# Kernel tuning notes

Measured on AMD Instinct MI355X. Metric: run time of the kernel, lower is better.

## Reference

```python
import jax, jax.numpy as jnp
import numpy as np

DIM = 1  # quantization axis (channels)


def setup_inputs() -> dict:
    key = jax.random.key(0)
    kx, kc = jax.random.split(key)
    x = jax.random.normal(kx, (32, 256, 32, 32), dtype=jnp.float32)
    # nn.init.normal_(weight, 0, 1.1)
    codebook = 1.1 * jax.random.normal(kc, (8192, 256), dtype=jnp.float32)
    return {"x": x, "codebook": codebook}


def reference(x, codebook):
    # move quantization dim to last: [B, C, H, W] -> [B, W, H, C]
    xt = jnp.swapaxes(x, -1, DIM)
    flat = xt.reshape(-1, xt.shape[-1])  # [N, D]
    # squared distances ||f - c||^2 = ||f||^2 - 2 f.c + ||c||^2  -> [N, K]
    d2 = (jnp.sum(flat * flat, axis=1, keepdims=True)
          - 2.0 * (flat @ codebook.T)
          + jnp.sum(codebook * codebook, axis=1))
    idx = jnp.argmin(d2, axis=1)                      # [N]
    codes = codebook[idx].reshape(xt.shape)           # nearest-code gather
    indices = idx.reshape(xt.shape[:-1])
    # transpose back to original layout
    codes = jnp.swapaxes(codes, -1, DIM)              # [B, C, H, W]
    indices = jnp.swapaxes(indices, -1, DIM)          # [B, H, W]
    return codes, indices
```

## Files before the change

kernel.cpp:

```cpp
#include <hip/hip_runtime.h>
#include <math.h>


typedef _Float16 v8h __attribute__((ext_vector_type(8)));
typedef float f32x16 __attribute__((ext_vector_type(16)));
typedef unsigned int u32;

#define MFMA16 __builtin_amdgcn_mfma_f32_32x32x16_f16

__device__ __forceinline__ void gll16(const _Float16* g, _Float16* l) {
  __builtin_amdgcn_global_load_lds(
      (const __attribute__((address_space(1))) void*)(const void*)g,
      (__attribute__((address_space(3))) void*)(void*)l, 16, 0, 0);
}

__global__ __launch_bounds__(256) void cnorm_k(const float4* __restrict__ cb4,
                                               float* __restrict__ cn) {
  int lane = threadIdx.x & 63;
  int row = (blockIdx.x << 2) + (threadIdx.x >> 6);
  float4 v = cb4[(size_t)row * 64 + lane];
  float s = v.x * v.x + v.y * v.y + v.z * v.z + v.w * v.w;
#pragma unroll
  for (int off = 32; off > 0; off >>= 1) s += __shfl_xor(s, off, 64);
  if (lane == 0) cn[row] = s;
}

__global__ __launch_bounds__(256) void split_cb(const float4* __restrict__ cb4,
                                                _Float16* __restrict__ W) {
  const int j = threadIdx.x & 31;
  const int ks = j >> 1, hi = j & 1;
  const int r = (blockIdx.x << 3) + (threadIdx.x >> 5);
  const float4* src = cb4 + (size_t)r * 64 + (ks << 2) + (hi << 1);
  float4 v0 = src[0], v1 = src[1];
  float t[8] = {v0.x, v0.y, v0.z, v0.w, v1.x, v1.y, v1.z, v1.w};
  v8h hv, mv;
#pragma unroll
  for (int i = 0; i < 8; ++i) {
    float vs = t[i] * 8192.f;
    _Float16 h = (_Float16)vs;
    _Float16 m = (_Float16)(vs - (float)h);
    hv[i] = h; mv[i] = m;
  }
  const int wv = (r >> 6) & 7, c64 = r & 63;
  _Float16* base = W + ((size_t)((r >> 9) << 4) + ks) * 16384 + (wv << 11);
  *(v8h*)(base + (hi << 9) + (c64 << 3)) = hv;
  *(v8h*)(base + 1024 + (hi << 9) + (c64 << 3)) = mv;
}

__global__ void __launch_bounds__(512, 1) vq_fast(const float* __restrict__ x,
                                                  const float4* __restrict__ cb4,
                                                  const float* __restrict__ cn,
                                                  const _Float16* __restrict__ W,
                                                  float* __restrict__ out) {
  __shared__ __align__(16) _Float16 F2[2][64][264];
  __shared__ __align__(16) _Float16 Bsh[2][16384];
  __shared__ float fnP[64][8];
  __shared__ float fnS[64];
  __shared__ float wredS[8][64];
  __shared__ u32  wredC[8][64];
  __shared__ u32  finS[64];

  const int tid = threadIdx.x;
  const int lane = tid & 63;
  const int w = tid >> 6;
  const int col = lane & 31;
  const int hi = lane >> 5;
  const int b = blockIdx.x >> 4;
  const int h0 = (blockIdx.x & 15) << 1;

  const int chunk = w << 11;
  const int rb0 = chunk + (hi << 9) + (col << 3);

  {
    const _Float16* src = W + chunk + (lane << 3);
#pragma unroll
    for (int i = 0; i < 4; ++i) gll16(src + (i << 9), &Bsh[0][chunk + (i << 9)]);
  }

  {
    const float* xb = x + ((size_t)b << 18) + (h0 << 5);
    float s = 0.f;
#pragma unroll
    for (int j = 0; j < 4; ++j) {
      v8h hv, mv;
#pragma unroll
      for (int i = 0; i < 8; ++i) {
        const int c = (w << 5) + (j << 3) + i;
        float v = xb[(size_t)c * 1024 + lane];
        s += v * v;
        float vs = v * 8192.f;
        _Float16 h = (_Float16)vs;
        _Float16 m = (_Float16)(vs - (float)h);
        hv[i] = h; mv[i] = m;
      }
      *(v8h*)&F2[0][lane][(w << 5) + (j << 3)] = hv;
      *(v8h*)&F2[1][lane][(w << 5) + (j << 3)] = mv;
    }
    fnP[lane][w] = s;
  }
  __syncthreads();
  if (tid < 64) {
    float t = 0.f;
#pragma unroll
    for (int j = 0; j < 8; ++j) t += fnP[tid][j];
    fnS[tid] = t;
  }
  __syncthreads();

  if (w >= 4) __builtin_amdgcn_s_sleep(15);

  float fnr[32];
#pragma unroll
  for (int sl = 0; sl < 32; ++sl) {
    const int row = ((sl >> 4) << 5) + (sl & 3) + (((sl >> 2) & 3) << 3) + (hi << 2);
    fnr[sl] = fnS[row];
  }

  f32x16 a00, a01, a10, a11;
#pragma unroll
  for (int r = 0; r < 16; ++r) { a00[r] = 0.f; a01[r] = 0.f; a10[r] = 0.f; a11[r] = 0.f; }
  float mn[32];
#pragma unroll
  for (int sl = 0; sl < 32; ++sl) mn[sl] = INFINITY;
  u32 idp[8] = {0, 0, 0, 0, 0, 0, 0, 0};
  float cnv0 = 0.f, cnv1 = 0.f;

#pragma unroll 1
  for (int ct = 0; ct < 16; ++ct) {
    if (w >= 4) __builtin_amdgcn_s_sleep(1);
#pragma unroll
    for (int ks = 0; ks < 16; ++ks) {
      const int st = (ct << 4) + ks;
      if (ks == 0) {
        cnv0 = cn[(ct << 9) + (w << 6) + col];
        cnv1 = cn[(ct << 9) + (w << 6) + 32 + col];
      }
      const bool more = (ct < 15) || (ks < 15);
      if (more) {
        const _Float16* src = W + ((size_t)(st + 1) << 14) + chunk + (lane << 3);
        _Float16* dst = &Bsh[(st + 1) & 1][chunk];
#pragma unroll
        for (int i = 0; i < 4; ++i) gll16(src + (i << 9), dst + (i << 9));
      }
      if (more) asm volatile("s_waitcnt vmcnt(4)" ::: "memory");
      else      asm volatile("s_waitcnt vmcnt(0)" ::: "memory");
      __builtin_amdgcn_sched_barrier(0);

      const int ko = (ks << 4) + (hi << 3);
      const v8h ah0 = *(const v8h*)&F2[0][col][ko];
      const v8h ah1 = *(const v8h*)&F2[0][32 + col][ko];
      const v8h am0 = *(const v8h*)&F2[1][col][ko];
      const v8h am1 = *(const v8h*)&F2[1][32 + col][ko];
      const _Float16* Bb = Bsh[st & 1];
      const v8h bh0 = *(const v8h*)&Bb[rb0];
      const v8h bh1 = *(const v8h*)&Bb[rb0 + 256];
      const v8h bm0 = *(const v8h*)&Bb[rb0 + 1024];
      const v8h bm1 = *(const v8h*)&Bb[rb0 + 1280];

      a00 = MFMA16(ah0, bh0, a00, 0, 0, 0);
      a01 = MFMA16(ah0, bh1, a01, 0, 0, 0);
      a10 = MFMA16(ah1, bh0, a10, 0, 0, 0);
      a11 = MFMA16(ah1, bh1, a11, 0, 0, 0);
      a00 = MFMA16(ah0, bm0, a00, 0, 0, 0);
      a01 = MFMA16(ah0, bm1, a01, 0, 0, 0);
      a10 = MFMA16(ah1, bm0, a10, 0, 0, 0);
      a11 = MFMA16(ah1, bm1, a11, 0, 0, 0);
      a00 = MFMA16(am0, bh0, a00, 0, 0, 0);
      a01 = MFMA16(am0, bh1, a01, 0, 0, 0);
      a10 = MFMA16(am1, bh0, a10, 0, 0, 0);
      a11 = MFMA16(am1, bh1, a11, 0, 0, 0);
    }
#pragma unroll
    for (int sl = 0; sl < 32; ++sl) {
      const int Mb = sl >> 4, reg = sl & 15;
      const float base = fnr[sl];
      const u32 sh = (u32)((sl & 3) << 3);
      {
        const float d = (Mb == 0) ? a00[reg] : a10[reg];
        float s = (base + (-0x1p-25f) * d) + cnv0;
        const bool better = s < mn[sl];
        const u32 curv = idp[sl >> 2];
        const u32 upd = (curv & ~(255u << sh)) | (((u32)(ct << 1)) << sh);
        idp[sl >> 2] = better ? upd : curv;
        mn[sl] = better ? s : mn[sl];
      }
      {
        const float d = (Mb == 0) ? a01[reg] : a11[reg];
        float s = (base + (-0x1p-25f) * d) + cnv1;
        const bool better = s < mn[sl];
        const u32 curv = idp[sl >> 2];
        const u32 upd = (curv & ~(255u << sh)) | (((u32)((ct << 1) | 1)) << sh);
        idp[sl >> 2] = better ? upd : curv;
        mn[sl] = better ? s : mn[sl];
      }
    }
#pragma unroll
    for (int r = 0; r < 16; ++r) { a00[r] = 0.f; a01[r] = 0.f; a10[r] = 0.f; a11[r] = 0.f; }
  }

#pragma unroll
  for (int sl = 0; sl < 32; ++sl) {
    float v = mn[sl];
    const u32 byte = (idp[sl >> 2] >> ((sl & 3) << 3)) & 255u;
    u32 code = ((byte >> 1) << 9) + ((u32)w << 6) + ((byte & 1) << 5) + (u32)col;
#pragma unroll
    for (int off = 1; off < 32; off <<= 1) {
      float v2 = __shfl_xor(v, off, 64);
      u32 c2 = (u32)__shfl_xor((int)code, off, 64);
      if (v2 < v || (v2 == v && c2 < code)) { v = v2; code = c2; }
    }
    if (col == 0) {
      const int row = ((sl >> 4) << 5) + (sl & 3) + (((sl >> 2) & 3) << 3) + (hi << 2);
      wredS[w][row] = v; wredC[w][row] = code;
    }
  }
  __syncthreads();
  if (tid < 64) {
    float bv = wredS[0][tid]; u32 bc = wredC[0][tid];
#pragma unroll
    for (int j = 1; j < 8; ++j) {
      float vv = wredS[j][tid]; u32 cc = wredC[j][tid];
      if (vv < bv || (vv == bv && cc < bc)) { bv = vv; bc = cc; }
    }
    finS[tid] = bc;
    out[(size_t)8388608 + ((size_t)b << 10) + (h0 << 5) + tid] = (float)bc;
  }
  __syncthreads();

  {
    const int pt = tid & 63, cg = tid >> 6;
    const u32 code = finS[pt];
    const float4* cbr = cb4 + ((size_t)code << 6);
    const size_t obase = ((size_t)b << 18) + (h0 << 5) + pt;
#pragma unroll
    for (int cc = 0; cc < 8; ++cc) {
      const int c4 = (cc << 3) + cg;
      float4 vv = cbr[c4];
      out[obase + (size_t)((c4 << 2) + 0) * 1024] = vv.x;
      out[obase + (size_t)((c4 << 2) + 1) * 1024] = vv.y;
      out[obase + (size_t)((c4 << 2) + 2) * 1024] = vv.z;
      out[obase + (size_t)((c4 << 2) + 3) * 1024] = vv.w;
    }
  }
}

__global__ void __launch_bounds__(512, 2) vq_fb(const float* __restrict__ x,
                                                const float4* __restrict__ cb4,
                                                const float* __restrict__ cn,
                                                float* __restrict__ out) {
  __shared__ __align__(16) _Float16 F2[2][64][264];
  __shared__ __align__(16) _Float16 Bsh[512][72];
  __shared__ float fnP[64][8];
  __shared__ float fnS[64];
  __shared__ float wredS[8][64];
  __shared__ u32  wredC[8][64];
  __shared__ u32  finS[64];

  const int tid = threadIdx.x;
  const int lane = tid & 63;
  const int w = tid >> 6;
  const int col = lane & 31;
  const int hi = lane >> 5;
  const int b = blockIdx.x >> 4;
  const int h0 = (blockIdx.x & 15) << 1;

  float4 rg[8];
  {
    const float4* src = cb4 + ((size_t)tid << 6);
#pragma unroll
    for (int j = 0; j < 8; ++j) rg[j] = src[j];
  }
  {
    const float* xb = x + ((size_t)b << 18) + (h0 << 5);
    float s = 0.f;
#pragma unroll
    for (int j = 0; j < 4; ++j) {
      v8h hv, mv;
#pragma unroll
      for (int i = 0; i < 8; ++i) {
        const int c = (w << 5) + (j << 3) + i;
        float v = xb[(size_t)c * 1024 + lane];
        s += v * v;
        float vs = v * 8192.f;
        _Float16 h = (_Float16)vs;
        _Float16 m = (_Float16)(vs - (float)h);
        hv[i] = h; mv[i] = m;
      }
      *(v8h*)&F2[0][lane][(w << 5) + (j << 3)] = hv;
      *(v8h*)&F2[1][lane][(w << 5) + (j << 3)] = mv;
    }
    fnP[lane][w] = s;
  }
  __syncthreads();
  if (tid < 64) {
    float t = 0.f;
#pragma unroll
    for (int j = 0; j < 8; ++j) t += fnP[tid][j];
    fnS[tid] = t;
  }
  {
#pragma unroll
    for (int j = 0; j < 4; ++j) {
      float t0[8] = {rg[2*j].x, rg[2*j].y, rg[2*j].z, rg[2*j].w,
                     rg[2*j+1].x, rg[2*j+1].y, rg[2*j+1].z, rg[2*j+1].w};
      v8h hv, mv;
#pragma unroll
      for (int i = 0; i < 8; ++i) {
        float vs = t0[i] * 8192.f;
        _Float16 h = (_Float16)vs;
        _Float16 m = (_Float16)(vs - (float)h);
        hv[i] = h; mv[i] = m;
      }
      *(v8h*)&Bsh[tid][(j << 3)] = hv;
      *(v8h*)&Bsh[tid][32 + (j << 3)] = mv;
    }
  }
  __syncthreads();

  float fnr[32];
#pragma unroll
  for (int sl = 0; sl < 32; ++sl) {
    const int row = ((sl >> 4) << 5) + (sl & 3) + (((sl >> 2) & 3) << 3) + (hi << 2);
    fnr[sl] = fnS[row];
  }

  f32x16 acc[2][2];
#pragma unroll
  for (int r = 0; r < 16; ++r) {
    acc[0][0][r] = 0.f; acc[0][1][r] = 0.f; acc[1][0][r] = 0.f; acc[1][1][r] = 0.f;
  }
  float mn[32];
#pragma unroll
  for (int sl = 0; sl < 32; ++sl) mn[sl] = INFINITY;
  u32 idp[8] = {0, 0, 0, 0, 0, 0, 0, 0};
  float cnv0 = 0.f, cnv1 = 0.f;

  for (int st = 0; st < 128; ++st) {
    const int ks = st & 7, ct = st >> 3;
    if (st < 127) {
      const int tn = st + 1;
      const float4* src = cb4 + ((size_t)((((tn >> 3) << 9) + tid)) << 6) + ((tn & 7) << 3);
#pragma unroll
      for (int j = 0; j < 8; ++j) rg[j] = src[j];
    }
    if (ks == 0) {
      cnv0 = cn[(ct << 9) + (w << 6) + col];
      cnv1 = cn[(ct << 9) + (w << 6) + 32 + col];
    }
    const int kb = ks << 5;
#pragma unroll
    for (int kh = 0; kh < 2; ++kh) {
      const int ko = kb + (kh << 4) + (hi << 3);
      const v8h ah0 = *(const v8h*)&F2[0][col][ko];
      const v8h ah1 = *(const v8h*)&F2[0][32 + col][ko];
      const v8h am0 = *(const v8h*)&F2[1][col][ko];
      const v8h am1 = *(const v8h*)&F2[1][32 + col][ko];
      const int bo = (kh << 4) + (hi << 3);
      const v8h bh0 = *(const v8h*)&Bsh[(w << 6) + col][bo];
      const v8h bh1 = *(const v8h*)&Bsh[(w << 6) + 32 + col][bo];
      const v8h bm0 = *(const v8h*)&Bsh[(w << 6) + col][32 + bo];
      const v8h bm1 = *(const v8h*)&Bsh[(w << 6) + 32 + col][32 + bo];
      acc[0][0] = MFMA16(ah0, bh0, acc[0][0], 0, 0, 0);
      acc[0][0] = MFMA16(ah0, bm0, acc[0][0], 0, 0, 0);
      acc[0][0] = MFMA16(am0, bh0, acc[0][0], 0, 0, 0);
      acc[0][1] = MFMA16(ah0, bh1, acc[0][1], 0, 0, 0);
      acc[0][1] = MFMA16(ah0, bm1, acc[0][1], 0, 0, 0);
      acc[0][1] = MFMA16(am0, bh1, acc[0][1], 0, 0, 0);
      acc[1][0] = MFMA16(ah1, bh0, acc[1][0], 0, 0, 0);
      acc[1][0] = MFMA16(ah1, bm0, acc[1][0], 0, 0, 0);
      acc[1][0] = MFMA16(am1, bh0, acc[1][0], 0, 0, 0);
      acc[1][1] = MFMA16(ah1, bh1, acc[1][1], 0, 0, 0);
      acc[1][1] = MFMA16(ah1, bm1, acc[1][1], 0, 0, 0);
      acc[1][1] = MFMA16(am1, bh1, acc[1][1], 0, 0, 0);
    }
    if (ks == 7) {
#pragma unroll
      for (int sl = 0; sl < 32; ++sl) {
        const int Mb = sl >> 4, reg = sl & 15;
        const float base = fnr[sl];
        const u32 sh = (u32)((sl & 3) << 3);
        {
          float s = (base + (-0x1p-25f) * acc[Mb][0][reg]) + cnv0;
          const bool better = s < mn[sl];
          const u32 curv = idp[sl >> 2];
          const u32 upd = (curv & ~(255u << sh)) | (((u32)(ct << 1)) << sh);
          idp[sl >> 2] = better ? upd : curv;
          mn[sl] = better ? s : mn[sl];
        }
        {
          float s = (base + (-0x1p-25f) * acc[Mb][1][reg]) + cnv1;
          const bool better = s < mn[sl];
          const u32 curv = idp[sl >> 2];
          const u32 upd = (curv & ~(255u << sh)) | (((u32)((ct << 1) | 1)) << sh);
          idp[sl >> 2] = better ? upd : curv;
          mn[sl] = better ? s : mn[sl];
        }
      }
#pragma unroll
      for (int r = 0; r < 16; ++r) {
        acc[0][0][r] = 0.f; acc[0][1][r] = 0.f; acc[1][0][r] = 0.f; acc[1][1][r] = 0.f;
      }
    }
    v8h cr[8];
    if (st < 127) {
#pragma unroll
      for (int j = 0; j < 4; ++j) {
        float t0[8] = {rg[2*j].x, rg[2*j].y, rg[2*j].z, rg[2*j].w,
                       rg[2*j+1].x, rg[2*j+1].y, rg[2*j+1].z, rg[2*j+1].w};
#pragma unroll
        for (int i = 0; i < 8; ++i) {
          float vs = t0[i] * 8192.f;
          _Float16 h = (_Float16)vs;
          _Float16 m = (_Float16)(vs - (float)h);
          cr[j][i] = h; cr[4 + j][i] = m;
        }
      }
    }
    __syncthreads();
    if (st < 127) {
#pragma unroll
      for (int j = 0; j < 4; ++j) {
        *(v8h*)&Bsh[tid][(j << 3)] = cr[j];
        *(v8h*)&Bsh[tid][32 + (j << 3)] = cr[4 + j];
      }
    }
    __syncthreads();
  }

#pragma unroll
  for (int sl = 0; sl < 32; ++sl) {
    float v = mn[sl];
    const u32 byte = (idp[sl >> 2] >> ((sl & 3) << 3)) & 255u;
    u32 code = ((byte >> 1) << 9) + ((u32)w << 6) + ((byte & 1) << 5) + (u32)col;
#pragma unroll
    for (int off = 1; off < 32; off <<= 1) {
      float v2 = __shfl_xor(v, off, 64);
      u32 c2 = (u32)__shfl_xor((int)code, off, 64);
      if (v2 < v || (v2 == v && c2 < code)) { v = v2; code = c2; }
    }
    if (col == 0) {
      const int row = ((sl >> 4) << 5) + (sl & 3) + (((sl >> 2) & 3) << 3) + (hi << 2);
      wredS[w][row] = v; wredC[w][row] = code;
    }
  }
  __syncthreads();
  if (tid < 64) {
    float bv = wredS[0][tid]; u32 bc = wredC[0][tid];
#pragma unroll
    for (int j = 1; j < 8; ++j) {
      float vv = wredS[j][tid]; u32 cc = wredC[j][tid];
      if (vv < bv || (vv == bv && cc < bc)) { bv = vv; bc = cc; }
    }
    finS[tid] = bc;
    out[(size_t)8388608 + ((size_t)b << 10) + (h0 << 5) + tid] = (float)bc;
  }
  __syncthreads();
  {
    const int pt = tid & 63, cg = tid >> 6;
    const u32 code = finS[pt];
    const float4* cbr = cb4 + ((size_t)code << 6);
    const size_t obase = ((size_t)b << 18) + (h0 << 5) + pt;
#pragma unroll
    for (int cc = 0; cc < 8; ++cc) {
      const int c4 = (cc << 3) + cg;
      float4 vv = cbr[c4];
      out[obase + (size_t)((c4 << 2) + 0) * 1024] = vv.x;
      out[obase + (size_t)((c4 << 2) + 1) * 1024] = vv.y;
      out[obase + (size_t)((c4 << 2) + 2) * 1024] = vv.z;
      out[obase + (size_t)((c4 << 2) + 3) * 1024] = vv.w;
    }
  }
}

extern "C" void kernel_launch(void* const* d_in, const int* in_sizes, int n_in,
                              void* d_out, int out_size, void* d_ws, size_t ws_size,
                              hipStream_t stream) {
  const float* x = (const float*)d_in[0];
  const float* cb = (const float*)d_in[1];
  float* out = (float*)d_out;
  float* cnorm = (float*)d_ws;

  cnorm_k<<<2048, 256, 0, stream>>>((const float4*)cb, cnorm);
  if (ws_size >= (size_t)32768 + (size_t)8388608) {
    _Float16* W = (_Float16*)((char*)d_ws + 32768);
    split_cb<<<1024, 256, 0, stream>>>((const float4*)cb, W);
    vq_fast<<<512, 512, 0, stream>>>(x, (const float4*)cb, cnorm, W, out);
  } else {
    vq_fb<<<512, 512, 0, stream>>>(x, (const float4*)cb, cnorm, out);
  }
}
```

Measured before the change: 441.7 us.

## Load two k-steps per stage into single LDS buffer, prefetch after register reads

Replaces the double-buffered LDS staging with a single buffer holding two k-steps. Each wave now reads its B fragments into registers first, then overwrites the same LDS region with the next two k-steps while it runs 24 MFMAs, and waits for the global-to-LDS loads at the end of each iteration. It also removes the s_sleep staggering of the upper waves. This halves the number of load and wait rounds and frees LDS, but exposes the full load latency at every iteration boundary, because the wait for the next tile comes right after the compute instead of one stage later.

```diff
diff --git a/kernel.cpp b/kernel.cpp
--- a/kernel.cpp
+++ b/kernel.cpp
@@ -53,7 +53,7 @@
                                                   const _Float16* __restrict__ W,
                                                   float* __restrict__ out) {
   __shared__ __align__(16) _Float16 F2[2][64][264];
-  __shared__ __align__(16) _Float16 Bsh[2][16384];
+  __shared__ __align__(16) _Float16 Bsh[32768];
   __shared__ float fnP[64][8];
   __shared__ float fnS[64];
   __shared__ float wredS[8][64];
@@ -72,9 +72,11 @@
   const int rb0 = chunk + (hi << 9) + (col << 3);
 
   {
-    const _Float16* src = W + chunk + (lane << 3);
-#pragma unroll
-    for (int i = 0; i < 4; ++i) gll16(src + (i << 9), &Bsh[0][chunk + (i << 9)]);
+    const _Float16* s0 = W + chunk + (lane << 3);
+#pragma unroll
+    for (int i = 0; i < 4; ++i) gll16(s0 + (i << 9), &Bsh[chunk + (i << 9)]);
+#pragma unroll
+    for (int i = 0; i < 4; ++i) gll16(s0 + 16384 + (i << 9), &Bsh[16384 + chunk + (i << 9)]);
   }
 
   {
@@ -107,8 +109,6 @@
   }
   __syncthreads();
 
-  if (w >= 4) __builtin_amdgcn_s_sleep(15);
-
   float fnr[32];
 #pragma unroll
   for (int sl = 0; sl < 32; ++sl) {
@@ -127,48 +127,71 @@
 
 #pragma unroll 1
   for (int ct = 0; ct < 16; ++ct) {
-    if (w >= 4) __builtin_amdgcn_s_sleep(1);
-#pragma unroll
-    for (int ks = 0; ks < 16; ++ks) {
-      const int st = (ct << 4) + ks;
-      if (ks == 0) {
+#pragma unroll
+    for (int u = 0; u < 8; ++u) {
+      const int t = (ct << 3) + u;
+      if (u == 0) {
         cnv0 = cn[(ct << 9) + (w << 6) + col];
         cnv1 = cn[(ct << 9) + (w << 6) + 32 + col];
       }
-      const bool more = (ct < 15) || (ks < 15);
-      if (more) {
-        const _Float16* src = W + ((size_t)(st + 1) << 14) + chunk + (lane << 3);
-        _Float16* dst = &Bsh[(st + 1) & 1][chunk];
-#pragma unroll
-        for (int i = 0; i < 4; ++i) gll16(src + (i << 9), dst + (i << 9));
-      }
-      if (more) asm volatile("s_waitcnt vmcnt(4)" ::: "memory");
-      else      asm volatile("s_waitcnt vmcnt(0)" ::: "memory");
+      const v8h b0h0 = *(const v8h*)&Bsh[rb0];
+      const v8h b0h1 = *(const v8h*)&Bsh[rb0 + 256];
+      const v8h b0m0 = *(const v8h*)&Bsh[rb0 + 1024];
+      const v8h b0m1 = *(const v8h*)&Bsh[rb0 + 1280];
+      const v8h b1h0 = *(const v8h*)&Bsh[16384 + rb0];
+      const v8h b1h1 = *(const v8h*)&Bsh[16384 + rb0 + 256];
+      const v8h b1m0 = *(const v8h*)&Bsh[16384 + rb0 + 1024];
+      const v8h b1m1 = *(const v8h*)&Bsh[16384 + rb0 + 1280];
+      asm volatile("s_waitcnt lgkmcnt(0)" ::: "memory");
       __builtin_amdgcn_sched_barrier(0);
-
-      const int ko = (ks << 4) + (hi << 3);
-      const v8h ah0 = *(const v8h*)&F2[0][col][ko];
-      const v8h ah1 = *(const v8h*)&F2[0][32 + col][ko];
-      const v8h am0 = *(const v8h*)&F2[1][col][ko];
-      const v8h am1 = *(const v8h*)&F2[1][32 + col][ko];
-      const _Float16* Bb = Bsh[st & 1];
-      const v8h bh0 = *(const v8h*)&Bb[rb0];
-      const v8h bh1 = *(const v8h*)&Bb[rb0 + 256];
-      const v8h bm0 = *(const v8h*)&Bb[rb0 + 1024];
-      const v8h bm1 = *(const v8h*)&Bb[rb0 + 1280];
-
-      a00 = MFMA16(ah0, bh0, a00, 0, 0, 0);
-      a01 = MFMA16(ah0, bh1, a01, 0, 0, 0);
-      a10 = MFMA16(ah1, bh0, a10, 0, 0, 0);
-      a11 = MFMA16(ah1, bh1, a11, 0, 0, 0);
-      a00 = MFMA16(ah0, bm0, a00, 0, 0, 0);
-      a01 = MFMA16(ah0, bm1, a01, 0, 0, 0);
-      a10 = MFMA16(ah1, bm0, a10, 0, 0, 0);
-      a11 = MFMA16(ah1, bm1, a11, 0, 0, 0);
-      a00 = MFMA16(am0, bh0, a00, 0, 0, 0);
-      a01 = MFMA16(am0, bh1, a01, 0, 0, 0);
-      a10 = MFMA16(am1, bh0, a10, 0, 0, 0);
-      a11 = MFMA16(am1, bh1, a11, 0, 0, 0);
+      if (t < 127) {
+        const _Float16* gsrc = W + ((size_t)(2 * t + 2) << 14) + chunk + (lane << 3);
+#pragma unroll
+        for (int i = 0; i < 4; ++i) gll16(gsrc + (i << 9), &Bsh[chunk + (i << 9)]);
+#pragma unroll
+        for (int i = 0; i < 4; ++i)
+          gll16(gsrc + 16384 + (i << 9), &Bsh[16384 + chunk + (i << 9)]);
+      }
+      {
+        const int ko = ((u << 1) << 4) + (hi << 3);
+        const v8h ah0 = *(const v8h*)&F2[0][col][ko];
+        const v8h ah1 = *(const v8h*)&F2[0][32 + col][ko];
+        const v8h am0 = *(const v8h*)&F2[1][col][ko];
+        const v8h am1 = *(const v8h*)&F2[1][32 + col][ko];
+        a00 = MFMA16(ah0, b0h0, a00, 0, 0, 0);
+        a01 = MFMA16(ah0, b0h1, a01, 0, 0, 0);
+        a10 = MFMA16(ah1, b0h0, a10, 0, 0, 0);
+        a11 = MFMA16(ah1, b0h1, a11, 0, 0, 0);
+        a00 = MFMA16(ah0, b0m0, a00, 0, 0, 0);
+        a01 = MFMA16(ah0, b0m1, a01, 0, 0, 0);
+        a10 = MFMA16(ah1, b0m0, a10, 0, 0, 0);
+        a11 = MFMA16(ah1, b0m1, a11, 0, 0, 0);
+        a00 = MFMA16(am0, b0h0, a00, 0, 0, 0);
+        a01 = MFMA16(am0, b0h1, a01, 0, 0, 0);
+        a10 = MFMA16(am1, b0h0, a10, 0, 0, 0);
+        a11 = MFMA16(am1, b0h1, a11, 0, 0, 0);
+      }
+      {
+        const int ko = (((u << 1) + 1) << 4) + (hi << 3);
+        const v8h ah0 = *(const v8h*)&F2[0][col][ko];
+        const v8h ah1 = *(const v8h*)&F2[0][32 + col][ko];
+        const v8h am0 = *(const v8h*)&F2[1][col][ko];
+        const v8h am1 = *(const v8h*)&F2[1][32 + col][ko];
+        a00 = MFMA16(ah0, b1h0, a00, 0, 0, 0);
+        a01 = MFMA16(ah0, b1h1, a01, 0, 0, 0);
+        a10 = MFMA16(ah1, b1h0, a10, 0, 0, 0);
+        a11 = MFMA16(ah1, b1h1, a11, 0, 0, 0);
+        a00 = MFMA16(ah0, b1m0, a00, 0, 0, 0);
+        a01 = MFMA16(ah0, b1m1, a01, 0, 0, 0);
+        a10 = MFMA16(ah1, b1m0, a10, 0, 0, 0);
+        a11 = MFMA16(ah1, b1m1, a11, 0, 0, 0);
+        a00 = MFMA16(am0, b1h0, a00, 0, 0, 0);
+        a01 = MFMA16(am0, b1h1, a01, 0, 0, 0);
+        a10 = MFMA16(am1, b1h0, a10, 0, 0, 0);
+        a11 = MFMA16(am1, b1h1, a11, 0, 0, 0);
+      }
+      asm volatile("s_waitcnt vmcnt(0)" ::: "memory");
+      __builtin_amdgcn_sched_barrier(0);
     }
 #pragma unroll
     for (int sl = 0; sl < 32; ++sl) {
```

New measurement: 440.8 us. About the same (-0.2%).
